# Optimization experiments

Hardware: AMD Instinct MI355X
Metric: run time of the kernel (lower is better)

## Reference

```python
import jax, jax.numpy as jnp
import numpy as np

SQRT_2_OVER_PI = 0.7978845608028654  # sqrt(2/pi)

def gelu_tanh(x):
    # F.gelu(x, approximate='tanh')
    return 0.5 * x * (1.0 + jnp.tanh(SQRT_2_OVER_PI * (x + 0.044715 * x * x * x)))

def setup_inputs() -> dict:
    key = jax.random.key(0)
    k1, k2, k3, k4 = jax.random.split(key, 4)
    B, S, DIN, DOUT = 8, 2048, 1152, 4608
    hidden_states = jax.random.normal(k1, (B, S, DIN), dtype=jnp.float32)
    # simulated int8 quantized weights (symmetric, per-output-channel scale)
    w_int8 = jax.random.randint(k2, (DOUT, DIN), -127, 128, dtype=jnp.int32)
    w_scale = jax.random.uniform(k3, (DOUT,), dtype=jnp.float32, minval=0.001, maxval=0.01)
    bias = jax.random.normal(k4, (DOUT,), dtype=jnp.float32) * 0.02
    return {"hidden_states": hidden_states, "w_int8": w_int8, "w_scale": w_scale, "bias": bias}

def reference(hidden_states, w_int8, w_scale, bias):
    # dequantize: per-output-channel scale
    w = w_int8.astype(hidden_states.dtype) * w_scale[:, None]  # [DOUT, DIN]
    # linear projection: [B,S,DIN] @ [DIN,DOUT] -> [B,S,DOUT]
    proj = jnp.einsum('bsd,od->bso', hidden_states, w) + bias
    return gelu_tanh(proj)
```

## Files before the change

### kernel.cpp

```cpp
#include <hip/hip_runtime.h>
#include <cstdint>
#include <cstddef>

#define M_DIM 16384
#define N_DIM 4608
#define K_DIM 1152

typedef __attribute__((ext_vector_type(8))) __bf16 bf16x8;
typedef __attribute__((ext_vector_type(4))) float  f32x4;
typedef __attribute__((ext_vector_type(4))) int    v4i;

__device__ __forceinline__ unsigned short f2bf(float f) {
    unsigned int u = __float_as_uint(f);
    unsigned int r = (u + 0x7FFFu + ((u >> 16) & 1u)) >> 16;
    return (unsigned short)r;
}

__device__ __forceinline__ float gelu_tanh_f(float v) {
    float u = 0.7978845608028654f * (v + 0.044715f * v * v * v);
    float a = fabsf(u);
    float t = __expf(-2.0f * a);
    float th = (1.0f - t) / (1.0f + t);
    th = (u < 0.0f) ? -th : th;
    return 0.5f * v * (1.0f + th);
}

#define QA_BLOCKS (M_DIM / 4)
#define W4_COUNT  ((N_DIM * K_DIM) / 4)
#define PW_BLOCKS ((W4_COUNT + 255) / 256)

__global__ void prepass(const float* __restrict__ A,
                        const int* __restrict__ w,
                        signed char* __restrict__ qa,
                        float* __restrict__ sA,
                        signed char* __restrict__ qw) {
    if (blockIdx.x < QA_BLOCKS) {
        const int lane = threadIdx.x & 63;
        const int row  = blockIdx.x * 4 + (threadIdx.x >> 6);
        const float2* src = (const float2*)(A + (size_t)row * K_DIM);
        float2 v[9];
        float amax = 0.f;
#pragma unroll
        for (int j = 0; j < 9; ++j) {
            v[j] = src[j * 64 + lane];
            amax = fmaxf(amax, fmaxf(fabsf(v[j].x), fabsf(v[j].y)));
        }
#pragma unroll
        for (int off = 32; off > 0; off >>= 1)
            amax = fmaxf(amax, __shfl_xor(amax, off));
        amax = fmaxf(amax, 1e-30f);
        float inv = 127.0f / amax;
        if (lane == 0) sA[row] = amax * (1.0f / 127.0f);
        char2* dst = (char2*)(qa + (size_t)row * K_DIM);
#pragma unroll
        for (int j = 0; j < 9; ++j) {
            char2 o;
            o.x = (signed char)__float2int_rn(v[j].x * inv);
            o.y = (signed char)__float2int_rn(v[j].y * inv);
            dst[j * 64 + lane] = o;
        }
    } else {
        int i = (blockIdx.x - QA_BLOCKS) * 256 + threadIdx.x;
        if (i >= W4_COUNT) return;
        int4 v = ((const int4*)w)[i];
        char4 o;
        o.x = (signed char)v.x; o.y = (signed char)v.y;
        o.z = (signed char)v.z; o.w = (signed char)v.w;
        ((char4*)qw)[i] = o;
    }
}

__global__ void qgelu_gemm_i8(const signed char* __restrict__ Aq,
                              const signed char* __restrict__ Wq,
                              const float* __restrict__ sA,
                              const float* __restrict__ w_scale,
                              const float* __restrict__ bias,
                              float* __restrict__ out) {
    __shared__ __align__(16) signed char As[128 * 128];
    __shared__ __align__(16) signed char Bs[128 * 128];

    const int tid    = threadIdx.x;
    const int l      = tid & 63;
    const int wv     = tid >> 6;
    const int lane16 = l & 15;
    const int quad   = l >> 4;
    const int m0 = blockIdx.x * 128;
    const int n0 = blockIdx.y * 128;
    const int wm = (wv & 1) * 64;
    const int wn = (wv >> 1) * 64;

    v4i acc[4][4];
#pragma unroll
    for (int i = 0; i < 4; ++i)
#pragma unroll
        for (int j = 0; j < 4; ++j) acc[i][j] = v4i{0, 0, 0, 0};

    for (int kt = 0; kt < K_DIM / 128; ++kt) {
        __syncthreads();
#pragma unroll
        for (int i = 0; i < 4; ++i) {
            int q   = wv * 64 + i * 256 + l;
            int row = q >> 3;
            int p   = q & 7;
            int c   = p ^ (row & 7);
            const signed char* ga = Aq + (size_t)(m0 + row) * K_DIM + kt * 128 + c * 16;
            const signed char* gb = Wq + (size_t)(n0 + row) * K_DIM + kt * 128 + c * 16;
            signed char* la = As + (size_t)(wv * 64 + i * 256) * 16;
            signed char* lb = Bs + (size_t)(wv * 64 + i * 256) * 16;
            __builtin_amdgcn_global_load_lds(
                (const __attribute__((address_space(1))) unsigned int*)ga,
                (__attribute__((address_space(3))) unsigned int*)la, 16, 0, 0);
            __builtin_amdgcn_global_load_lds(
                (const __attribute__((address_space(1))) unsigned int*)gb,
                (__attribute__((address_space(3))) unsigned int*)lb, 16, 0, 0);
        }
        __syncthreads();

#pragma unroll
        for (int s = 0; s < 2; ++s) {
            v4i af[4], bfr[4];
#pragma unroll
            for (int mt = 0; mt < 4; ++mt) {
                int row = wm + mt * 16 + lane16;
                int p   = (s * 4 + quad) ^ (row & 7);
                af[mt]  = *(const v4i*)(As + row * 128 + p * 16);
            }
#pragma unroll
            for (int nt = 0; nt < 4; ++nt) {
                int row = wn + nt * 16 + lane16;
                int p   = (s * 4 + quad) ^ (row & 7);
                bfr[nt] = *(const v4i*)(Bs + row * 128 + p * 16);
            }
#pragma unroll
            for (int mt = 0; mt < 4; ++mt)
#pragma unroll
                for (int nt = 0; nt < 4; ++nt)
                    acc[mt][nt] = __builtin_amdgcn_mfma_i32_16x16x64_i8(
                        af[mt], bfr[nt], acc[mt][nt], 0, 0, 0);
        }
    }

#pragma unroll
    for (int nt = 0; nt < 4; ++nt) {
        int n    = n0 + wn + nt * 16 + lane16;
        float sc = w_scale[n];
        float bi = bias[n];
#pragma unroll
        for (int mt = 0; mt < 4; ++mt) {
            int mbase = m0 + wm + mt * 16 + quad * 4;
#pragma unroll
            for (int r = 0; r < 4; ++r) {
                float v = (float)acc[mt][nt][r] * sA[mbase + r] * sc + bi;
                __builtin_nontemporal_store(
                    gelu_tanh_f(v), &out[(size_t)(mbase + r) * N_DIM + n]);
            }
        }
    }
}

__global__ void qgelu_gemm_bf16_fused(const float* __restrict__ Af,
                                      const int* __restrict__ Wi,
                                      const float* __restrict__ w_scale,
                                      const float* __restrict__ bias,
                                      float* __restrict__ out) {
    __shared__ __align__(16) unsigned short As[128 * 64];
    __shared__ __align__(16) unsigned short Bs[128 * 64];

    const int tid    = threadIdx.x;
    const int l      = tid & 63;
    const int wv     = tid >> 6;
    const int lane16 = l & 15;
    const int quad   = l >> 4;
    const int m0 = blockIdx.x * 128;
    const int n0 = blockIdx.y * 128;
    const int wm = (wv & 1) * 64;
    const int wn = (wv >> 1) * 64;

    f32x4 acc[4][4];
#pragma unroll
    for (int i = 0; i < 4; ++i)
#pragma unroll
        for (int j = 0; j < 4; ++j) acc[i][j] = f32x4{0.f, 0.f, 0.f, 0.f};

    for (int kt = 0; kt < K_DIM / 64; ++kt) {
        __syncthreads();
#pragma unroll
        for (int i = 0; i < 8; ++i) {
            int g    = i * 256 + tid;
            int row  = g >> 4;
            int grp  = g & 15;
            int c    = grp >> 1;
            int half = g & 1;
            int p    = c ^ (row & 7);
            int off  = row * 64 + p * 8 + half * 4;
            {
                float4 v = *(const float4*)(Af + (size_t)(m0 + row) * K_DIM + kt * 64 + grp * 4);
                ushort4 o;
                o.x = f2bf(v.x); o.y = f2bf(v.y); o.z = f2bf(v.z); o.w = f2bf(v.w);
                *(ushort4*)(As + off) = o;
            }
            {
                int4 v = *(const int4*)(Wi + (size_t)(n0 + row) * K_DIM + kt * 64 + grp * 4);
                ushort4 o;
                o.x = f2bf((float)v.x); o.y = f2bf((float)v.y);
                o.z = f2bf((float)v.z); o.w = f2bf((float)v.w);
                *(ushort4*)(Bs + off) = o;
            }
        }
        __syncthreads();

#pragma unroll
        for (int s = 0; s < 2; ++s) {
            bf16x8 af[4], bfr[4];
#pragma unroll
            for (int mt = 0; mt < 4; ++mt) {
                int row = wm + mt * 16 + lane16;
                int p   = (s * 4 + quad) ^ (row & 7);
                af[mt]  = *(const bf16x8*)(As + row * 64 + p * 8);
            }
#pragma unroll
            for (int nt = 0; nt < 4; ++nt) {
                int row = wn + nt * 16 + lane16;
                int p   = (s * 4 + quad) ^ (row & 7);
                bfr[nt] = *(const bf16x8*)(Bs + row * 64 + p * 8);
            }
#pragma unroll
            for (int mt = 0; mt < 4; ++mt)
#pragma unroll
                for (int nt = 0; nt < 4; ++nt)
                    acc[mt][nt] = __builtin_amdgcn_mfma_f32_16x16x32_bf16(
                        af[mt], bfr[nt], acc[mt][nt], 0, 0, 0);
        }
    }

#pragma unroll
    for (int nt = 0; nt < 4; ++nt) {
        int n    = n0 + wn + nt * 16 + lane16;
        float sc = w_scale[n];
        float bi = bias[n];
#pragma unroll
        for (int mt = 0; mt < 4; ++mt) {
#pragma unroll
            for (int r = 0; r < 4; ++r) {
                int m   = m0 + wm + mt * 16 + quad * 4 + r;
                float v = acc[mt][nt][r] * sc + bi;
                __builtin_nontemporal_store(
                    gelu_tanh_f(v), &out[(size_t)m * N_DIM + n]);
            }
        }
    }
}

extern "C" void kernel_launch(void* const* d_in, const int* in_sizes, int n_in,
                              void* d_out, int out_size, void* d_ws, size_t ws_size,
                              hipStream_t stream) {
    const float* hs   = (const float*)d_in[0];
    const int*   w8   = (const int*)d_in[1];
    const float* wsc  = (const float*)d_in[2];
    const float* bias = (const float*)d_in[3];
    float* out = (float*)d_out;

    const size_t nA = (size_t)M_DIM * K_DIM;
    const size_t nW = (size_t)N_DIM * K_DIM;
    const size_t need = nA + nW + (size_t)M_DIM * sizeof(float);

    dim3 grid(M_DIM / 128, N_DIM / 128);

    if (ws_size >= need) {
        signed char* qa = (signed char*)d_ws;
        signed char* qw = qa + nA;
        float* sA = (float*)(qa + nA + nW);
        prepass<<<QA_BLOCKS + PW_BLOCKS, 256, 0, stream>>>(hs, w8, qa, sA, qw);
        qgelu_gemm_i8<<<grid, 256, 0, stream>>>(qa, qw, sA, wsc, bias, out);
    } else {
        qgelu_gemm_bf16_fused<<<grid, 256, 0, stream>>>(hs, w8, wsc, bias, out);
    }
}
```

Before: 458.6 us.

## Replace int8 GEMM with 256x256-tile, 8-wave, double-buffered phased pipeline

```diff
diff --git a/kernel.cpp b/kernel.cpp
--- a/kernel.cpp
+++ b/kernel.cpp
@@ -5,6 +5,7 @@
 #define M_DIM 16384
 #define N_DIM 4608
 #define K_DIM 1152
+#define NKT   (K_DIM / 128)
 
 typedef __attribute__((ext_vector_type(8))) __bf16 bf16x8;
 typedef __attribute__((ext_vector_type(4))) float  f32x4;
@@ -70,92 +71,155 @@
     }
 }
 
-__global__ void qgelu_gemm_i8(const signed char* __restrict__ Aq,
-                              const signed char* __restrict__ Wq,
-                              const float* __restrict__ sA,
-                              const float* __restrict__ w_scale,
-                              const float* __restrict__ bias,
-                              float* __restrict__ out) {
-    __shared__ __align__(16) signed char As[128 * 128];
-    __shared__ __align__(16) signed char Bs[128 * 128];
+
+template <int MH, int NH>
+__device__ __forceinline__ void mfma_quad(v4i (&acc)[2][4][2][2],
+                                          v4i (&a)[4][2],
+                                          v4i (&b)[2][2][2]) {
+    __builtin_amdgcn_s_setprio(1);
+#pragma unroll
+    for (int s = 0; s < 2; ++s)
+#pragma unroll
+        for (int mt = 0; mt < 4; ++mt)
+#pragma unroll
+            for (int nt = 0; nt < 2; ++nt)
+                acc[MH][mt][NH][nt] = __builtin_amdgcn_mfma_i32_16x16x64_i8(
+                    a[mt][s], b[NH][nt][s], acc[MH][mt][NH][nt], 0, 0, 0);
+    __builtin_amdgcn_s_setprio(0);
+}
+
+__global__ __launch_bounds__(512, 2) void qgemm_i8_8phase(
+    const signed char* __restrict__ Aq,
+    const signed char* __restrict__ Wq,
+    const float* __restrict__ sA,
+    const float* __restrict__ w_scale,
+    const float* __restrict__ bias,
+    float* __restrict__ out) {
+    __shared__ __align__(16) signed char lds[2][2][256 * 128];
 
     const int tid    = threadIdx.x;
     const int l      = tid & 63;
     const int wv     = tid >> 6;
     const int lane16 = l & 15;
     const int quad   = l >> 4;
-    const int m0 = blockIdx.x * 128;
-    const int n0 = blockIdx.y * 128;
-    const int wm = (wv & 1) * 64;
+
+    const int bid = blockIdx.x;
+    const int swz = (bid & 7) * (1152 / 8) + (bid >> 3);
+    const int mt0 = (swz / 18) * 256;
+    const int nt0 = (swz % 18) * 256;
+
+    const int wm = (wv & 1) * 128;
     const int wn = (wv >> 1) * 64;
 
-    v4i acc[4][4];
-#pragma unroll
-    for (int i = 0; i < 4; ++i)
-#pragma unroll
-        for (int j = 0; j < 4; ++j) acc[i][j] = v4i{0, 0, 0, 0};
-
-    for (int kt = 0; kt < K_DIM / 128; ++kt) {
-        __syncthreads();
-#pragma unroll
-        for (int i = 0; i < 4; ++i) {
-            int q   = wv * 64 + i * 256 + l;
-            int row = q >> 3;
-            int p   = q & 7;
-            int c   = p ^ (row & 7);
-            const signed char* ga = Aq + (size_t)(m0 + row) * K_DIM + kt * 128 + c * 16;
-            const signed char* gb = Wq + (size_t)(n0 + row) * K_DIM + kt * 128 + c * 16;
-            signed char* la = As + (size_t)(wv * 64 + i * 256) * 16;
-            signed char* lb = Bs + (size_t)(wv * 64 + i * 256) * 16;
+    auto stage_half = [&](int buf, int mat, int half, int kt) {
+        const signed char* gbase =
+            (mat == 0) ? (Aq + (size_t)mt0 * K_DIM) : (Wq + (size_t)nt0 * K_DIM);
+#pragma unroll
+        for (int j = 0; j < 2; ++j) {
+            int q   = j * 512 + tid;
+            int row = half * 128 + (q >> 3);
+            int c   = (q & 7) ^ (row & 7);
+            const signed char* g = gbase + (size_t)row * K_DIM + kt * 128 + c * 16;
+            signed char* d = &lds[buf][mat][half * 16384 + (j * 512 + wv * 64) * 16];
             __builtin_amdgcn_global_load_lds(
-                (const __attribute__((address_space(1))) unsigned int*)ga,
-                (__attribute__((address_space(3))) unsigned int*)la, 16, 0, 0);
-            __builtin_amdgcn_global_load_lds(
-                (const __attribute__((address_space(1))) unsigned int*)gb,
-                (__attribute__((address_space(3))) unsigned int*)lb, 16, 0, 0);
-        }
-        __syncthreads();
-
-#pragma unroll
-        for (int s = 0; s < 2; ++s) {
-            v4i af[4], bfr[4];
-#pragma unroll
-            for (int mt = 0; mt < 4; ++mt) {
-                int row = wm + mt * 16 + lane16;
-                int p   = (s * 4 + quad) ^ (row & 7);
-                af[mt]  = *(const v4i*)(As + row * 128 + p * 16);
-            }
-#pragma unroll
-            for (int nt = 0; nt < 4; ++nt) {
-                int row = wn + nt * 16 + lane16;
-                int p   = (s * 4 + quad) ^ (row & 7);
-                bfr[nt] = *(const v4i*)(Bs + row * 128 + p * 16);
-            }
-#pragma unroll
-            for (int mt = 0; mt < 4; ++mt)
-#pragma unroll
-                for (int nt = 0; nt < 4; ++nt)
-                    acc[mt][nt] = __builtin_amdgcn_mfma_i32_16x16x64_i8(
-                        af[mt], bfr[nt], acc[mt][nt], 0, 0, 0);
-        }
-    }
-
-#pragma unroll
-    for (int nt = 0; nt < 4; ++nt) {
-        int n    = n0 + wn + nt * 16 + lane16;
-        float sc = w_scale[n];
-        float bi = bias[n];
-#pragma unroll
-        for (int mt = 0; mt < 4; ++mt) {
-            int mbase = m0 + wm + mt * 16 + quad * 4;
-#pragma unroll
-            for (int r = 0; r < 4; ++r) {
-                float v = (float)acc[mt][nt][r] * sA[mbase + r] * sc + bi;
-                __builtin_nontemporal_store(
-                    gelu_tanh_f(v), &out[(size_t)(mbase + r) * N_DIM + n]);
-            }
-        }
-    }
+                (const __attribute__((address_space(1))) unsigned int*)g,
+                (__attribute__((address_space(3))) unsigned int*)d, 16, 0, 0);
+        }
+    };
+
+    v4i acc[2][4][2][2];
+#pragma unroll
+    for (int mh = 0; mh < 2; ++mh)
+#pragma unroll
+        for (int mt = 0; mt < 4; ++mt)
+#pragma unroll
+            for (int nh = 0; nh < 2; ++nh)
+#pragma unroll
+                for (int nt = 0; nt < 2; ++nt)
+                    acc[mh][mt][nh][nt] = v4i{0, 0, 0, 0};
+
+    v4i a[4][2];
+    v4i b[2][2][2];
+
+    auto ldA = [&](int cur, int mh, int mt, int s) -> v4i {
+        int r = wm + mh * 64 + mt * 16 + lane16;
+        int p = (s * 4 + quad) ^ (r & 7);
+        return *(const v4i*)&lds[cur][0][r * 128 + p * 16];
+    };
+    auto ldB = [&](int cur, int nh, int nt, int s) -> v4i {
+        int r = wn + nh * 32 + nt * 16 + lane16;
+        int p = (s * 4 + quad) ^ (r & 7);
+        return *(const v4i*)&lds[cur][1][r * 128 + p * 16];
+    };
+
+    stage_half(0, 0, 0, 0); stage_half(0, 0, 1, 0);
+    stage_half(0, 1, 0, 0); stage_half(0, 1, 1, 0);
+    stage_half(1, 1, 0, 1); stage_half(1, 1, 1, 1);
+    asm volatile("s_waitcnt vmcnt(4)" ::: "memory");
+    __builtin_amdgcn_sched_barrier(0);
+    __builtin_amdgcn_s_barrier();
+
+    for (int kt = 0; kt < NKT; ++kt) {
+        const int cur = kt & 1, nxt = cur ^ 1;
+#pragma unroll
+        for (int mt = 0; mt < 4; ++mt)
+#pragma unroll
+            for (int s = 0; s < 2; ++s) a[mt][s] = ldA(cur, 0, mt, s);
+#pragma unroll
+        for (int nt = 0; nt < 2; ++nt)
+#pragma unroll
+            for (int s = 0; s < 2; ++s) b[0][nt][s] = ldB(cur, 0, nt, s);
+        if (kt + 1 < NKT) stage_half(nxt, 0, 0, kt + 1);
+        __builtin_amdgcn_s_barrier();
+        mfma_quad<0, 0>(acc, a, b);
+        __builtin_amdgcn_s_barrier();
+#pragma unroll
+        for (int nt = 0; nt < 2; ++nt)
+#pragma unroll
+            for (int s = 0; s < 2; ++s) b[1][nt][s] = ldB(cur, 1, nt, s);
+        if (kt + 1 < NKT) stage_half(nxt, 0, 1, kt + 1);
+        __builtin_amdgcn_s_barrier();
+        mfma_quad<0, 1>(acc, a, b);
+        __builtin_amdgcn_s_barrier();
+#pragma unroll
+        for (int mt = 0; mt < 4; ++mt)
+#pragma unroll
+            for (int s = 0; s < 2; ++s) a[mt][s] = ldA(cur, 1, mt, s);
+        if (kt + 2 < NKT) stage_half(cur, 1, 0, kt + 2);
+        __builtin_amdgcn_s_barrier();
+        mfma_quad<1, 1>(acc, a, b);
+        __builtin_amdgcn_s_barrier();
+        if (kt + 2 < NKT) stage_half(cur, 1, 1, kt + 2);
+        mfma_quad<1, 0>(acc, a, b);
+        if (kt + 2 < NKT) {
+            asm volatile("s_waitcnt vmcnt(4)" ::: "memory");
+        } else if (kt + 1 < NKT) {
+            asm volatile("s_waitcnt vmcnt(0)" ::: "memory");
+        }
+        __builtin_amdgcn_sched_barrier(0);
+        __builtin_amdgcn_s_barrier();
+    }
+
+#pragma unroll
+    for (int nh = 0; nh < 2; ++nh)
+#pragma unroll
+        for (int nt = 0; nt < 2; ++nt) {
+            int n    = nt0 + wn + nh * 32 + nt * 16 + lane16;
+            float sc = w_scale[n];
+            float bi = bias[n];
+#pragma unroll
+            for (int mh = 0; mh < 2; ++mh)
+#pragma unroll
+                for (int mt = 0; mt < 4; ++mt) {
+                    int mbase = mt0 + wm + mh * 64 + mt * 16 + quad * 4;
+#pragma unroll
+                    for (int r = 0; r < 4; ++r) {
+                        float v = (float)acc[mh][mt][nh][nt][r] * sA[mbase + r] * sc + bi;
+                        __builtin_nontemporal_store(
+                            gelu_tanh_f(v), &out[(size_t)(mbase + r) * N_DIM + n]);
+                    }
+                }
+        }
 }
 
 __global__ void qgelu_gemm_bf16_fused(const float* __restrict__ Af,
@@ -264,15 +328,15 @@
     const size_t nW = (size_t)N_DIM * K_DIM;
     const size_t need = nA + nW + (size_t)M_DIM * sizeof(float);
 
-    dim3 grid(M_DIM / 128, N_DIM / 128);
-
     if (ws_size >= need) {
         signed char* qa = (signed char*)d_ws;
         signed char* qw = qa + nA;
         float* sA = (float*)(qa + nA + nW);
         prepass<<<QA_BLOCKS + PW_BLOCKS, 256, 0, stream>>>(hs, w8, qa, sA, qw);
-        qgelu_gemm_i8<<<grid, 256, 0, stream>>>(qa, qw, sA, wsc, bias, out);
+        qgemm_i8_8phase<<<dim3((M_DIM / 256) * (N_DIM / 256)), 512, 0, stream>>>(
+            qa, qw, sA, wsc, bias, out);
     } else {
+        dim3 grid(M_DIM / 128, N_DIM / 128);
         qgelu_gemm_bf16_fused<<<grid, 256, 0, stream>>>(hs, w8, wsc, bias, out);
     }
 }
```

Measured after the change: 460.4 us. About the same (+0.4%).

## Double-buffer int8 GEMM K-loop, swizzle tile order, and stage epilogue through LDS

Applied to the files above, without the earlier changes.

```diff
diff --git a/kernel.cpp b/kernel.cpp
--- a/kernel.cpp
+++ b/kernel.cpp
@@ -5,6 +5,7 @@
 #define M_DIM 16384
 #define N_DIM 4608
 #define K_DIM 1152
+#define NKT64 (K_DIM / 64)
 
 typedef __attribute__((ext_vector_type(8))) __bf16 bf16x8;
 typedef __attribute__((ext_vector_type(4))) float  f32x4;
@@ -17,12 +18,10 @@
 }
 
 __device__ __forceinline__ float gelu_tanh_f(float v) {
-    float u = 0.7978845608028654f * (v + 0.044715f * v * v * v);
-    float a = fabsf(u);
-    float t = __expf(-2.0f * a);
-    float th = (1.0f - t) / (1.0f + t);
-    th = (u < 0.0f) ? -th : th;
-    return 0.5f * v * (1.0f + th);
+    float v2 = v * v;
+    float u2 = v * fmaf(v2, 0.07135481627260093f, 1.5957691216057308f);
+    float e  = __expf(-u2);
+    return v / (1.0f + e);
 }
 
 #define QA_BLOCKS (M_DIM / 4)
@@ -70,91 +69,133 @@
     }
 }
 
-__global__ void qgelu_gemm_i8(const signed char* __restrict__ Aq,
-                              const signed char* __restrict__ Wq,
-                              const float* __restrict__ sA,
-                              const float* __restrict__ w_scale,
-                              const float* __restrict__ bias,
-                              float* __restrict__ out) {
-    __shared__ __align__(16) signed char As[128 * 128];
-    __shared__ __align__(16) signed char Bs[128 * 128];
+
+__global__ __launch_bounds__(256, 3) void qgemm_i8_128(
+    const signed char* __restrict__ Aq,
+    const signed char* __restrict__ Wq,
+    const float* __restrict__ sA,
+    const float* __restrict__ w_scale,
+    const float* __restrict__ bias,
+    float* __restrict__ out) {
+    __shared__ __align__(16) signed char As[2][128 * 64];
+    __shared__ __align__(16) signed char Bs[2][128 * 64];
 
     const int tid    = threadIdx.x;
     const int l      = tid & 63;
     const int wv     = tid >> 6;
     const int lane16 = l & 15;
     const int quad   = l >> 4;
-    const int m0 = blockIdx.x * 128;
-    const int n0 = blockIdx.y * 128;
+
+    const int bid = blockIdx.x;
+    const int swz = (bid & 7) * (4608 / 8) + (bid >> 3);
+    const int m0  = (swz / 36) * 128;
+    const int n0  = (swz % 36) * 128;
+
     const int wm = (wv & 1) * 64;
     const int wn = (wv >> 1) * 64;
 
+    auto stage = [&](int buf, int kt) {
+#pragma unroll
+        for (int j = 0; j < 2; ++j) {
+            int q   = j * 256 + tid;
+            int row = q >> 2;
+            int c   = (q & 3) ^ (row & 3);
+            const signed char* gA = Aq + (size_t)(m0 + row) * K_DIM + kt * 64 + c * 16;
+            const signed char* gB = Wq + (size_t)(n0 + row) * K_DIM + kt * 64 + c * 16;
+            __builtin_amdgcn_global_load_lds(
+                (const __attribute__((address_space(1))) unsigned int*)gA,
+                (__attribute__((address_space(3))) unsigned int*)&As[buf][q * 16], 16, 0, 0);
+            __builtin_amdgcn_global_load_lds(
+                (const __attribute__((address_space(1))) unsigned int*)gB,
+                (__attribute__((address_space(3))) unsigned int*)&Bs[buf][q * 16], 16, 0, 0);
+        }
+    };
+
     v4i acc[4][4];
 #pragma unroll
     for (int i = 0; i < 4; ++i)
 #pragma unroll
         for (int j = 0; j < 4; ++j) acc[i][j] = v4i{0, 0, 0, 0};
 
-    for (int kt = 0; kt < K_DIM / 128; ++kt) {
-        __syncthreads();
-#pragma unroll
-        for (int i = 0; i < 4; ++i) {
-            int q   = wv * 64 + i * 256 + l;
-            int row = q >> 3;
-            int p   = q & 7;
-            int c   = p ^ (row & 7);
-            const signed char* ga = Aq + (size_t)(m0 + row) * K_DIM + kt * 128 + c * 16;
-            const signed char* gb = Wq + (size_t)(n0 + row) * K_DIM + kt * 128 + c * 16;
-            signed char* la = As + (size_t)(wv * 64 + i * 256) * 16;
-            signed char* lb = Bs + (size_t)(wv * 64 + i * 256) * 16;
-            __builtin_amdgcn_global_load_lds(
-                (const __attribute__((address_space(1))) unsigned int*)ga,
-                (__attribute__((address_space(3))) unsigned int*)la, 16, 0, 0);
-            __builtin_amdgcn_global_load_lds(
-                (const __attribute__((address_space(1))) unsigned int*)gb,
-                (__attribute__((address_space(3))) unsigned int*)lb, 16, 0, 0);
-        }
-        __syncthreads();
-
-#pragma unroll
-        for (int s = 0; s < 2; ++s) {
-            v4i af[4], bfr[4];
-#pragma unroll
-            for (int mt = 0; mt < 4; ++mt) {
-                int row = wm + mt * 16 + lane16;
-                int p   = (s * 4 + quad) ^ (row & 7);
-                af[mt]  = *(const v4i*)(As + row * 128 + p * 16);
-            }
-#pragma unroll
-            for (int nt = 0; nt < 4; ++nt) {
-                int row = wn + nt * 16 + lane16;
-                int p   = (s * 4 + quad) ^ (row & 7);
-                bfr[nt] = *(const v4i*)(Bs + row * 128 + p * 16);
-            }
-#pragma unroll
-            for (int mt = 0; mt < 4; ++mt)
-#pragma unroll
-                for (int nt = 0; nt < 4; ++nt)
-                    acc[mt][nt] = __builtin_amdgcn_mfma_i32_16x16x64_i8(
-                        af[mt], bfr[nt], acc[mt][nt], 0, 0, 0);
-        }
-    }
-
+    stage(0, 0);
+
+    for (int kt = 0; kt < NKT64; ++kt) {
+        const int cur = kt & 1;
+        if (kt + 1 < NKT64) {
+            stage(cur ^ 1, kt + 1);
+            asm volatile("s_waitcnt vmcnt(4)" ::: "memory");
+        } else {
+            asm volatile("s_waitcnt vmcnt(0)" ::: "memory");
+        }
+        __builtin_amdgcn_sched_barrier(0);
+        __builtin_amdgcn_s_barrier();
+
+        v4i a[4], b[4];
+#pragma unroll
+        for (int mt = 0; mt < 4; ++mt) {
+            int r = wm + mt * 16 + lane16;
+            int p = quad ^ (r & 3);
+            a[mt] = *(const v4i*)&As[cur][r * 64 + p * 16];
+        }
+#pragma unroll
+        for (int nt = 0; nt < 4; ++nt) {
+            int r = wn + nt * 16 + lane16;
+            int p = quad ^ (r & 3);
+            b[nt] = *(const v4i*)&Bs[cur][r * 64 + p * 16];
+        }
+        __builtin_amdgcn_s_setprio(1);
+#pragma unroll
+        for (int mt = 0; mt < 4; ++mt)
+#pragma unroll
+            for (int nt = 0; nt < 4; ++nt)
+                acc[mt][nt] = __builtin_amdgcn_mfma_i32_16x16x64_i8(
+                    a[mt], b[nt], acc[mt][nt], 0, 0, 0);
+        __builtin_amdgcn_s_setprio(0);
+        __builtin_amdgcn_s_barrier();
+    }
+
+    __syncthreads();
+
+    float sc4[4], bi4[4];
 #pragma unroll
     for (int nt = 0; nt < 4; ++nt) {
-        int n    = n0 + wn + nt * 16 + lane16;
-        float sc = w_scale[n];
-        float bi = bias[n];
-#pragma unroll
-        for (int mt = 0; mt < 4; ++mt) {
-            int mbase = m0 + wm + mt * 16 + quad * 4;
+        int n = n0 + wn + nt * 16 + lane16;
+        sc4[nt] = w_scale[n];
+        bi4[nt] = bias[n];
+    }
+
+    float* scr = (float*)(&As[0][0]) + wv * 1024;
+    const int lo3 = lane16 & 3;
+
+#pragma unroll
+    for (int mt = 0; mt < 4; ++mt) {
+        const int rbase = m0 + wm + mt * 16;
+        const f32x4 sa = *(const f32x4*)(sA + rbase + quad * 4);
+#pragma unroll
+        for (int nt = 0; nt < 4; ++nt) {
+            const int col   = nt * 16 + lane16;
+            const int chunk = col >> 2;
 #pragma unroll
             for (int r = 0; r < 4; ++r) {
-                float v = (float)acc[mt][nt][r] * sA[mbase + r] * sc + bi;
-                __builtin_nontemporal_store(
-                    gelu_tanh_f(v), &out[(size_t)(mbase + r) * N_DIM + n]);
-            }
-        }
+                const int row16 = quad * 4 + r;
+                const int c2    = chunk ^ row16;
+                float v = (float)acc[mt][nt][r] * sa[r] * sc4[nt] + bi4[nt];
+                scr[row16 * 64 + c2 * 4 + lo3] = gelu_tanh_f(v);
+            }
+        }
+        asm volatile("s_waitcnt lgkmcnt(0)" ::: "memory");
+        __builtin_amdgcn_sched_barrier(0);
+#pragma unroll
+        for (int s = 0; s < 4; ++s) {
+            const int row16 = s * 4 + quad;
+            const int c2    = lane16 ^ row16;
+            f32x4 val = *(const f32x4*)(scr + row16 * 64 + c2 * 4);
+            __builtin_nontemporal_store(
+                val, (f32x4*)(out + (size_t)(rbase + row16) * N_DIM
+                              + n0 + wn + lane16 * 4));
+        }
+        asm volatile("s_waitcnt lgkmcnt(0)" ::: "memory");
+        __builtin_amdgcn_sched_barrier(0);
     }
 }
 
@@ -264,15 +305,15 @@
     const size_t nW = (size_t)N_DIM * K_DIM;
     const size_t need = nA + nW + (size_t)M_DIM * sizeof(float);
 
-    dim3 grid(M_DIM / 128, N_DIM / 128);
-
     if (ws_size >= need) {
         signed char* qa = (signed char*)d_ws;
         signed char* qw = qa + nA;
         float* sA = (float*)(qa + nA + nW);
         prepass<<<QA_BLOCKS + PW_BLOCKS, 256, 0, stream>>>(hs, w8, qa, sA, qw);
-        qgelu_gemm_i8<<<grid, 256, 0, stream>>>(qa, qw, sA, wsc, bias, out);
+        qgemm_i8_128<<<dim3((M_DIM / 128) * (N_DIM / 128)), 256, 0, stream>>>(
+            qa, qw, sA, wsc, bias, out);
     } else {
+        dim3 grid(M_DIM / 128, N_DIM / 128);
         qgelu_gemm_bf16_fused<<<grid, 256, 0, stream>>>(hs, w8, wsc, bias, out);
     }
 }
```

Result: no change. 453.3 us (-1.2%).
